# Performance work log

Hardware: AMD Instinct MI355X
Metric: run time of the kernel (lower is better)

The kernel has to match this reference:

```python
import jax, jax.numpy as jnp
import numpy as np

EPS = 1e-8
MIN_VAL = -1e7  # module default min_val=-10000000.0


def _div_safe(n, d):
    return n / jnp.maximum(d, EPS)


def _cosine_pairwise(v1, v2):
    # v1: (B,L1,H), v2: (B,L2,H) -> (B,L1,L2)
    n1 = jnp.linalg.norm(v1, axis=2, keepdims=True)
    n2 = jnp.linalg.norm(v2, axis=2, keepdims=True)
    a = jnp.einsum('bik,bjk->bij', v1, v2)
    return _div_safe(a, n1 * jnp.swapaxes(n2, 1, 2))


def _masked_max(v, mask, axis, keepdims=False):
    rep = jnp.where(mask > 0, v, MIN_VAL)
    val = jnp.max(rep, axis=axis, keepdims=keepdims)
    m = jnp.max(jnp.broadcast_to(mask, v.shape), axis=axis, keepdims=keepdims)
    return val * m


def _masked_mean(v, mask, axis, keepdims=False):
    s = jnp.sum(v * mask, axis=axis, keepdims=keepdims)
    c = jnp.sum(jnp.broadcast_to(mask, v.shape), axis=axis, keepdims=keepdims)
    return _div_safe(s, c)


def _cos_sim(a, b, axis):
    # torch F.cosine_similarity semantics: dot / (max(|a|,eps)*max(|b|,eps))
    dot = jnp.sum(a * b, axis=axis)
    na = jnp.maximum(jnp.linalg.norm(a, axis=axis), EPS)
    nb = jnp.maximum(jnp.linalg.norm(b, axis=axis), EPS)
    return dot / (na * nb)


def _mpm(v1, v2, w):
    # v1, v2: (B,L,H); w: (P,H) -> ((B,L,1), (B,L,P))
    mv1 = _cos_sim(v1, v2, 2)[..., None]
    v1w = w[None, None] * v1[:, :, None, :]  # (B,L,P,H)
    v2w = w[None, None] * v2[:, :, None, :]
    return mv1, _cos_sim(v1w, v2w, 3)


def _mpm_pairwise(v1, v2, w):
    # v1: (B,L1,H), v2: (B,L2,H), w: (P,H) -> (B,L1,L2,P)
    v1w = w[None, :, None, :] * v1[:, None, :, :]  # (B,P,L1,H)
    v2w = w[None, :, None, :] * v2[:, None, :, :]  # (B,P,L2,H)
    n1 = jnp.linalg.norm(v1w, axis=3, keepdims=True)
    n2 = jnp.linalg.norm(v2w, axis=3, keepdims=True)
    n = jnp.einsum('bpik,bpjk->bpij', v1w, v2w)
    d = n1 * jnp.swapaxes(n2, 2, 3)
    return jnp.transpose(_div_safe(n, d), (0, 2, 3, 1))


def setup_inputs() -> dict:
    key = jax.random.key(0)
    ks = jax.random.split(key, 8)
    B, L, H, P = 32, 128, 100, 20
    return {
        'context_p': jax.random.normal(ks[0], (B, L, H), dtype=jnp.float32),
        'mask_p': jax.random.randint(ks[1], (B, L), 0, 2, dtype=jnp.int32),
        'context_h': jax.random.normal(ks[2], (B, L, H), dtype=jnp.float32),
        'mask_h': jax.random.randint(ks[3], (B, L), 0, 2, dtype=jnp.int32),
        'w0': jax.random.uniform(ks[4], (P, H), dtype=jnp.float32),
        'w1': jax.random.uniform(ks[5], (P, H), dtype=jnp.float32),
        'w2': jax.random.uniform(ks[6], (P, H), dtype=jnp.float32),
        'w3': jax.random.uniform(ks[7], (P, H), dtype=jnp.float32),
    }


def reference(context_p, mask_p, context_h, mask_h, w0, w1, w2, w3):
    mask_p = mask_p.astype(jnp.float32)
    mask_h = mask_h.astype(jnp.float32)
    B, Lp, H = context_p.shape
    Lh = context_h.shape[1]

    mask_p_h = mask_p[:, :, None] * mask_h[:, None, :]   # (B,Lp,Lh)
    mask_h_p = jnp.swapaxes(mask_p_h, 1, 2)              # (B,Lh,Lp)
    cp = context_p * mask_p[..., None]
    ch = context_h * mask_h[..., None]

    # --- pairwise cosine + masked max/mean pooling ---
    cos = _cosine_pairwise(cp, ch)                        # (B,Lp,Lh)
    cosT = jnp.swapaxes(cos, 1, 2)
    cos_max_p = _masked_max(cos, mask_p_h, 2, True)
    cos_mean_p = _masked_mean(cos, mask_p_h, 2, True)
    cos_max_h = _masked_max(cosT, mask_h_p, 2, True)
    cos_mean_h = _masked_mean(cosT, mask_h_p, 2, True)

    # --- full match (is_forward=True: last real token) ---
    idx_p = jnp.clip(jnp.sum(mask_p, 1).astype(jnp.int32) - 1, 0)[:, None, None]
    idx_h = jnp.clip(jnp.sum(mask_h, 1).astype(jnp.int32) - 1, 0)[:, None, None]
    cp_last = jnp.take_along_axis(cp, jnp.broadcast_to(idx_p, (B, 1, H)), axis=1)
    ch_last = jnp.take_along_axis(ch, jnp.broadcast_to(idx_h, (B, 1, H)), axis=1)
    mv_p_f1, mv_p_fP = _mpm(cp, jnp.broadcast_to(ch_last, (B, Lp, H)), w0)
    mv_h_f1, mv_h_fP = _mpm(ch, jnp.broadcast_to(cp_last, (B, Lh, H)), w0)

    # --- maxpool match ---
    mv_max = _mpm_pairwise(cp, ch, w1)                    # (B,Lp,Lh,P)
    mv_p_max = _masked_max(mv_max, mask_p_h[..., None], 2)
    mv_p_mean = _masked_mean(mv_max, mask_p_h[..., None], 2)
    mv_maxT = jnp.transpose(mv_max, (0, 2, 1, 3))
    mv_h_max = _masked_max(mv_maxT, mask_h_p[..., None], 2)
    mv_h_mean = _masked_mean(mv_maxT, mask_h_p[..., None], 2)

    # --- attentive match (mean) ---
    att_mean_h = _div_safe(jnp.einsum('bij,bjh->bih', cos, ch),
                           jnp.sum(cos, 2, keepdims=True))
    att_mean_p = _div_safe(jnp.einsum('bij,bih->bjh', cos, cp),
                           jnp.swapaxes(jnp.sum(cos, 1, keepdims=True), 1, 2))
    mv_p_am1, mv_p_amP = _mpm(cp, att_mean_h, w2)
    mv_h_am1, mv_h_amP = _mpm(ch, att_mean_p, w2)

    # --- max-attentive match ---
    att_h = ch[:, None, :, :] * cos[:, :, :, None]        # (B,Lp,Lh,H)
    att_p_t = cp[:, None, :, :] * cosT[:, :, :, None]     # (B,Lh,Lp,H) == att_p.permute(0,2,1,3)
    att_max_h = _masked_max(att_h, mask_p_h[..., None], 2)
    att_max_p = _masked_max(att_p_t, mask_h_p[..., None], 2)
    mv_p_ax1, mv_p_axP = _mpm(cp, att_max_h, w3)
    mv_h_ax1, mv_h_axP = _mpm(ch, att_max_p, w3)

    mv_p = jnp.concatenate([cos_max_p, cos_mean_p, mv_p_f1, mv_p_fP,
                            mv_p_max, mv_p_mean, mv_p_am1, mv_p_amP,
                            mv_p_ax1, mv_p_axP], axis=2)
    mv_h = jnp.concatenate([cos_max_h, cos_mean_h, mv_h_f1, mv_h_fP,
                            mv_h_max, mv_h_mean, mv_h_am1, mv_h_amP,
                            mv_h_ax1, mv_h_axP], axis=2)
    return mv_p, mv_h
```

## Files before the change

kernel.cpp:

```cpp
#include <hip/hip_runtime.h>
#include <math.h>


namespace {
constexpr int B = 32;
constexpr int L = 128;
constexpr int H = 100;
constexpr int P = 20;
constexpr int C = 105;
constexpr int TI = 8;
constexpr int SMEM_BYTES = 50176;
constexpr float EPSF = 1e-8f;
constexpr float MINV = -1e7f;
}

typedef unsigned short u16;
typedef unsigned int u32;
typedef short sh8 __attribute__((ext_vector_type(8)));
typedef float f4 __attribute__((ext_vector_type(4)));

__device__ __forceinline__ u16 f2bf(float f) {
    u32 u = __float_as_uint(f);
    u += 0x7FFFu + ((u >> 16) & 1u);
    return (u16)(u >> 16);
}
__device__ __forceinline__ float bf2f(u32 h) {
    return __uint_as_float(h << 16);
}
__device__ __forceinline__ u32 pack2(float a, float b) {
    return (u32)f2bf(a) | ((u32)f2bf(b) << 16);
}

__global__ void k_prep(const float* __restrict__ ctx_p, const int* __restrict__ mask_p,
                       const float* __restrict__ ctx_h, const int* __restrict__ mask_h,
                       const float* __restrict__ w1,
                       float* __restrict__ cp, float* __restrict__ ch,
                       u16* __restrict__ cpb, u16* __restrict__ chb,
                       float* __restrict__ np_, float* __restrict__ nh_,
                       float* __restrict__ nwp, float* __restrict__ nwh)
{
    const int b = blockIdx.y, i = blockIdx.x, side = blockIdx.z, t = threadIdx.x;
    const float* ctx = side ? ctx_h : ctx_p;
    const int*  mask = side ? mask_h : mask_p;
    float* dst  = side ? ch  : cp;
    u16*   dstb = side ? chb : cpb;
    float* nrm  = side ? nh_ : np_;
    float* nw   = side ? nwh : nwp;

    const int row = b * L + i;
    __shared__ __align__(16) float sv2[H];
    const float m = (float)mask[row];
    float v = 0.f;
    if (t < H) {
        v = ctx[row * H + t] * m;
        dst[row * H + t] = v;
        sv2[t] = v * v;
    }
    dstb[row * 128 + t] = f2bf(v);
    __syncthreads();

    const int w = t >> 6, ln = t & 63;
    int g = -1, seg = 0;
    if (w == 0) { if (ln < 60) { g = ln / 5; seg = ln % 5; } }
    else        { if (ln < 45) { g = 12 + ln / 5; seg = ln % 5; } }
    if (g >= 0) {
        const float4* v4 = (const float4*)sv2;
        float acc = 0.f;
        if (g < P) {
            const float4* w4 = (const float4*)(w1 + g * H);
            #pragma unroll
            for (int k = seg * 5; k < seg * 5 + 5; ++k) {
                float4 wv_ = w4[k], s = v4[k];
                acc += wv_.x * wv_.x * s.x + wv_.y * wv_.y * s.y +
                       wv_.z * wv_.z * s.z + wv_.w * wv_.w * s.w;
            }
        } else {
            #pragma unroll
            for (int k = seg * 5; k < seg * 5 + 5; ++k) {
                float4 s = v4[k];
                acc += s.x + s.y + s.z + s.w;
            }
        }
        float a1 = __shfl(acc, ln + 1), a2 = __shfl(acc, ln + 2);
        float a3 = __shfl(acc, ln + 3), a4 = __shfl(acc, ln + 4);
        if (seg == 0) {
            float s = acc + a1 + a2 + a3 + a4;
            if (g < P) nw[row * P + g] = sqrtf(s);
            else       nrm[row] = sqrtf(s);
        }
    }
}

__global__ __launch_bounds__(512) void
k_main(const float* __restrict__ cp, const float* __restrict__ ch,
       const u16* __restrict__ cpb, const u16* __restrict__ chb,
       const float* __restrict__ np_, const float* __restrict__ nh_,
       const float* __restrict__ nw1p, const float* __restrict__ nw1h,
       const int* __restrict__ mask_p, const int* __restrict__ mask_h,
       const float* __restrict__ w0, const float* __restrict__ w1,
       const float* __restrict__ w2, const float* __restrict__ w3,
       float* __restrict__ out)
{
    __shared__ __align__(16) char smem[SMEM_BYTES];
    const int bx = blockIdx.x, b = blockIdx.y, t = threadIdx.x;
    const int wv = t >> 6, ln = t & 63;
    float* out_p = out;
    float* out_h = out + (size_t)B * L * C;

    if (bx < P) {
        const int p = bx;
        u16*  sB    = (u16*)smem;
        float* snwA = (float*)(smem + 34816);
        float* snwB = (float*)(smem + 35328);
        float* smA  = (float*)(smem + 35840);
        float* smB  = (float*)(smem + 36352);
        float* pJmax= (float*)(smem + 36864);
        float* pJsum= (float*)(smem + 37376);
        float* pImax= (float*)(smem + 37888);
        float* pIsum= (float*)(smem + 41984);
        float* sRed = (float*)(smem + 46080);

        if (t < 128) {
            snwA[t] = nw1p[(b * L + t) * P + p];
            snwB[t] = nw1h[(b * L + t) * P + p];
            smA[t] = (float)mask_p[b * L + t];
            smB[t] = (float)mask_h[b * L + t];
        }
        __syncthreads();

        if (t < 64) {
            float a0 = smB[t], a1 = smB[t + 64];
            float mx = fmaxf(a0, a1), sm = a0 + a1;
            for (int d = 1; d < 64; d <<= 1) {
                mx = fmaxf(mx, __shfl_xor(mx, d));
                sm += __shfl_xor(sm, d);
            }
            if (t == 0) { sRed[2] = mx; sRed[3] = sm; }
        } else if (t < 128) {
            const int l = t - 64;
            float a0 = smA[l], a1 = smA[l + 64];
            float mx = fmaxf(a0, a1), sm = a0 + a1;
            for (int d = 1; d < 64; d <<= 1) {
                mx = fmaxf(mx, __shfl_xor(mx, d));
                sm += __shfl_xor(sm, d);
            }
            if (l == 0) { sRed[0] = mx; sRed[1] = sm; }
        }

        {
            const uint4* src = (const uint4*)(chb + (size_t)b * L * 128);
            #pragma unroll
            for (int it = 0; it < 4; ++it) {
                int idx = it * 512 + t;
                int row = idx >> 4, kc = (idx & 15) * 8;
                uint4 v = src[idx];
                *(uint4*)&sB[row * 136 + kc] = v;
            }
        }
        __syncthreads();

        const int m = ln & 15, q = ln >> 4;

        float swv[4][8];
        #pragma unroll
        for (int ks = 0; ks < 4; ++ks)
            #pragma unroll
            for (int e = 0; e < 8; ++e) {
                int k = ks * 32 + q * 8 + e;
                float w = (k < H) ? w1[p * H + k] : 0.f;
                swv[ks][e] = w * w;
            }

        f4 acc[8];
        #pragma unroll
        for (int ct = 0; ct < 8; ++ct) acc[ct] = (f4){0.f, 0.f, 0.f, 0.f};

        const uint4* gA = (const uint4*)(cpb + (size_t)(b * L + wv * 16 + m) * 128);

        #pragma unroll
        for (int ks = 0; ks < 4; ++ks) {
            uint4 va = gA[ks * 4 + q];
            sh8 af;
            {
                u32 vs[4] = {va.x, va.y, va.z, va.w};
                u32 r[4];
                #pragma unroll
                for (int e = 0; e < 4; ++e) {
                    float f0 = bf2f(vs[e] & 0xffffu) * swv[ks][2 * e];
                    float f1 = bf2f(vs[e] >> 16) * swv[ks][2 * e + 1];
                    r[e] = (u32)f2bf(f0) | ((u32)f2bf(f1) << 16);
                }
                uint4 o = {r[0], r[1], r[2], r[3]};
                af = __builtin_bit_cast(sh8, o);
            }
            const int ko = ks * 32 + q * 8;
            #pragma unroll
            for (int ct = 0; ct < 8; ++ct) {
                sh8 bb = *(const sh8*)&sB[(ct * 16 + m) * 136 + ko];
                acc[ct] = __builtin_amdgcn_mfma_f32_16x16x32_bf16(af, bb, acc[ct], 0, 0, 0);
            }
        }

        float nB[8], mBv[8], imax[8], isum[8];
        #pragma unroll
        for (int ct = 0; ct < 8; ++ct) {
            const int j = ct * 16 + m;
            nB[ct] = snwB[j]; mBv[ct] = smB[j];
            imax[ct] = MINV; isum[ct] = 0.f;
        }
        #pragma unroll
        for (int reg = 0; reg < 4; ++reg) {
            const int i = wv * 16 + q * 4 + reg;
            const float na = snwA[i];
            const float ma = smA[i];
            float jmax = MINV, jsum = 0.f;
            #pragma unroll
            for (int ct = 0; ct < 8; ++ct) {
                float v = acc[ct][reg] *
                          __builtin_amdgcn_rcpf(fmaxf(na * nB[ct], EPSF));
                jmax = fmaxf(jmax, mBv[ct] > 0.f ? v : MINV);
                jsum += mBv[ct] > 0.f ? v : 0.f;
                imax[ct] = fmaxf(imax[ct], ma > 0.f ? v : MINV);
                isum[ct] += ma > 0.f ? v : 0.f;
            }
            for (int d = 1; d < 16; d <<= 1) {
                jmax = fmaxf(jmax, __shfl_xor(jmax, d));
                jsum += __shfl_xor(jsum, d);
            }
            if (m == 0) { pJmax[i] = jmax; pJsum[i] = jsum; }
        }
        #pragma unroll
        for (int ct = 0; ct < 8; ++ct) {
            float mx = imax[ct], sm = isum[ct];
            mx = fmaxf(mx, __shfl_xor(mx, 16)); sm += __shfl_xor(sm, 16);
            mx = fmaxf(mx, __shfl_xor(mx, 32)); sm += __shfl_xor(sm, 32);
            if (q == 0) { const int j = ct * 16 + m; pImax[wv * 128 + j] = mx; pIsum[wv * 128 + j] = sm; }
        }
        __syncthreads();

        if (t < 128) {
            const int i = t;
            const float ma = smA[i];
            const float mm = ma * sRed[2];
            const float cnt = ma * sRed[3];
            float* orow = out_p + ((size_t)b * L + i) * C;
            orow[23 + p] = pJmax[i] * mm;
            orow[43 + p] = ma * pJsum[i] / fmaxf(cnt, EPSF);

            const float mb = smB[i];
            float hmax = MINV, hsum = 0.f;
            #pragma unroll
            for (int s = 0; s < 8; ++s) {
                hmax = fmaxf(hmax, pImax[s * 128 + i]);
                hsum += pIsum[s * 128 + i];
            }
            float* hrow = out_h + ((size_t)b * L + i) * C;
            hrow[23 + p] = hmax * mb * sRed[0];
            hrow[43 + p] = mb * hsum / fmaxf(mb * sRed[1], EPSF);
        }
    } else {
        const int e = bx - P;
        const int side = e >> 4, tile = e & 15;
        const int i0 = tile * TI;
        const float* A   = side ? ch : cp;
        const float* Bv  = side ? cp : ch;
        const u16*  Ab16 = side ? chb : cpb;
        const u16*  Bvb  = side ? cpb : chb;
        const float* nA_ = side ? nh_ : np_;
        const float* nB_ = side ? np_ : nh_;
        const int* maskA = side ? mask_h : mask_p;
        const int* maskB = side ? mask_p : mask_h;
        float* outBase = out + ((size_t)side * B * L + (size_t)b * L) * C;

        float* scosC = (float*)(smem + 34816);
        float* sa    = (float*)(smem + 38912);
        float* sam   = (float*)(smem + 42496);
        float* sax   = (float*)(smem + 46080);
        float* sl    = (float*)(smem + 49664);
        float* snB   = (float*)(smem + 42496);
        float* snA   = (float*)(smem + 43008);
        u16*  cidx  = (u16*)(smem + 43040);
        int*   pnv   = (int*)(smem + 50112);

        scosC[t] = 0.f;
        scosC[t + 512] = 0.f;
        if (wv == 0) {
            int m0 = maskB[b * L + ln], m1 = maskB[b * L + 64 + ln];
            unsigned long long b0 = __ballot(m0 > 0);
            unsigned long long b1 = __ballot(m1 > 0);
            unsigned long long pre = (1ull << ln) - 1ull;
            int n0 = __popcll(b0);
            if (m0 > 0) cidx[__popcll(b0 & pre)] = (u16)ln;
            if (m1 > 0) cidx[n0 + __popcll(b1 & pre)] = (u16)(64 + ln);
            if (ln == 0) *pnv = n0 + __popcll(b1);
        } else if (wv >= 2) {
            for (int x = t - 128; x < TI * 128; x += 384) {
                int il = x >> 7, k = x & 127;
                if (k < H) sa[il * 112 + k] = A[((size_t)b * L + i0 + il) * H + k];
            }
        }
        __syncthreads();
        const int nv = *pnv;
        const int nct = (nv + 15) >> 4;

        {
            const uint4* src = (const uint4*)(Bvb + (size_t)b * L * 128);
            for (int c = t; c < nct * 256; c += 512) {
                int jj = c >> 4, cc = c & 15;
                uint4 v;
                if (jj < nv) v = src[(int)cidx[jj] * 16 + cc];
                else { v.x = v.y = v.z = v.w = 0u; }
                *(uint4*)(smem + jj * 272 + cc * 16) = v;
            }
            if (t < 128) snB[t] = (t < nv) ? nB_[b * L + (int)cidx[t]] : 0.f;
            else if (t < 136) snA[t - 128] = nA_[b * L + i0 + (t - 128)];
            if (wv == 1) {
                int last = nv - 1; if (last < 0) last = 0;
                const float* lr = Bv + ((size_t)b * L + last) * H;
                sl[ln] = lr[ln];
                if (ln + 64 < H) sl[ln + 64] = lr[ln + 64];
            }
        }
        __syncthreads();

        const int m = ln & 15, q = ln >> 4;
        if (wv < nct) {
            const uint4* gA = (const uint4*)(Ab16 + (size_t)(b * L + i0 + (m & 7)) * 128);
            f4 acc0 = (f4){0.f, 0.f, 0.f, 0.f};
            #pragma unroll
            for (int ks = 0; ks < 4; ++ks) {
                uint4 va = gA[ks * 4 + q];
                if (m >= 8) { va.x = va.y = va.z = va.w = 0u; }
                sh8 af = __builtin_bit_cast(sh8, va);
                const int ko2 = (ks * 32 + q * 8) * 2;
                sh8 bb = *(const sh8*)(smem + (wv * 16 + m) * 272 + ko2);
                acc0 = __builtin_amdgcn_mfma_f32_16x16x32_bf16(af, bb, acc0, 0, 0, 0);
            }
            if (q < 2) {
                #pragma unroll
                for (int reg = 0; reg < 4; ++reg) {
                    const int i = q * 4 + reg;
                    const int jj = wv * 16 + m;
                    scosC[i * 128 + jj] = acc0[reg] *
                        __builtin_amdgcn_rcpf(fmaxf(snA[i] * snB[jj], EPSF));
                }
            }
        }
        __syncthreads();

        {
            const int il = wv;
            const int gi = i0 + il;
            const float mA = (float)maskA[b * L + gi];
            float c0 = scosC[il * 128 + ln], c1 = scosC[il * 128 + 64 + ln];
            float scj = c0 + c1;
            float mv0 = (ln < nv) ? c0 : MINV;
            float mv1 = (ln + 64 < nv) ? c1 : MINV;
            float cmx = fmaxf(mv0, mv1);
            for (int d = 1; d < 64; d <<= 1) {
                scj += __shfl_xor(scj, d);
                cmx = fmaxf(cmx, __shfl_xor(cmx, d));
            }
            const float mm = (nv > 0) ? mA : 0.f;
            if (ln == 0) {
                float* orow = outBase + (size_t)gi * C;
                orow[0] = cmx * mm;
                orow[1] = mA * scj / fmaxf(mA * (float)nv, EPSF);
            }
            if (ln < 50) {
                float am0 = 0.f, am1 = 0.f, ax0 = MINV, ax1 = MINV;
                const u32* bp = (const u32*)smem + ln;
                const float* cr = scosC + il * 128;
                #pragma unroll 4
                for (int jj = 0; jj < nv; ++jj) {
                    u32 pk = bp[jj * 68];
                    float cj = cr[jj];
                    float v0 = cj * __uint_as_float(pk << 16);
                    float v1 = cj * __uint_as_float(pk & 0xffff0000u);
                    am0 += v0; am1 += v1;
                    ax0 = fmaxf(ax0, v0); ax1 = fmaxf(ax1, v1);
                }
                const float rs = __builtin_amdgcn_rcpf(fmaxf(scj, EPSF));
                sam[il * 112 + 2 * ln] = am0 * rs; sam[il * 112 + 2 * ln + 1] = am1 * rs;
                sax[il * 112 + 2 * ln] = ax0 * mm; sax[il * 112 + 2 * ln + 1] = ax1 * mm;
            }
        }
        __syncthreads();

        for (int idx = t; idx < 8 * 8 * 17; idx += 512) {
            int kc = (idx % 17) * 8;
            int tmp = idx / 17;
            int il = tmp >> 3, col = tmp & 7;
            const float* sa_il  = sa  + il * 112;
            const float* sam_il = sam + il * 112;
            const float* sax_il = sax + il * 112;
            const float* p1 = (col >= 4) ? (col == 4 ? sl : col == 5 ? sam_il : sax_il)
                                         : sa_il;
            const float* p2 = (col == 0 || col == 4) ? sl :
                              (col == 1 || col == 5) ? sam_il :
                              (col == 2 || col == 6) ? sax_il : sa_il;
            u32 ow[4];
            #pragma unroll
            for (int e2 = 0; e2 < 4; ++e2) {
                int k0 = kc + 2 * e2;
                float f0 = (col < 7 && k0 < H)     ? p1[k0] * p2[k0]         : 0.f;
                float f1 = (col < 7 && k0 + 1 < H) ? p1[k0 + 1] * p2[k0 + 1] : 0.f;
                ow[e2] = pack2(f0, f1);
            }
            uint4 o = {ow[0], ow[1], ow[2], ow[3]};
            *(uint4*)(smem + (tmp * 136 + kc) * 2) = o;
        }
        for (int idx = t; idx < 64 * 17; idx += 512) {
            int kc = (idx % 17) * 8;
            int row = idx / 17;
            u32 ow[4];
            #pragma unroll
            for (int e2 = 0; e2 < 4; ++e2) {
                int k0 = kc + 2 * e2;
                float f0 = 0.f, f1 = 0.f;
                if (row < 60) {
                    const float* wr = (row < 20) ? w0 + row * H :
                                      (row < 40) ? w2 + (row - 20) * H :
                                                   w3 + (row - 40) * H;
                    if (k0 < H)     { float w = wr[k0];     f0 = w * w; }
                    if (k0 + 1 < H) { float w = wr[k0 + 1]; f1 = w * w; }
                } else if (row == 60) {
                    f0 = (k0 < H) ? 1.f : 0.f;
                    f1 = (k0 + 1 < H) ? 1.f : 0.f;
                }
                ow[e2] = pack2(f0, f1);
            }
            uint4 o = {ow[0], ow[1], ow[2], ow[3]};
            *(uint4*)(smem + 17408 + (row * 136 + kc) * 2) = o;
        }
        __syncthreads();

        f4 d3[4];
        #pragma unroll
        for (int Mt = 0; Mt < 4; ++Mt) d3[Mt] = (f4){0.f, 0.f, 0.f, 0.f};
        {
            const int cn = m & 7;
            #pragma unroll
            for (int ks = 0; ks < 4; ++ks) {
                const int ko2 = (ks * 32 + q * 8) * 2;
                sh8 bb = *(const sh8*)(smem + ((wv * 8 + cn) * 136) * 2 + ko2);
                #pragma unroll
                for (int Mt = 0; Mt < 4; ++Mt) {
                    sh8 aa = *(const sh8*)(smem + 17408 + ((Mt * 16 + m) * 136) * 2 + ko2);
                    d3[Mt] = __builtin_amdgcn_mfma_f32_16x16x32_bf16(aa, bb, d3[Mt], 0, 0, 0);
                }
            }
        }
        __syncthreads();

        if (m < 8) {
            #pragma unroll
            for (int Mt = 0; Mt < 4; ++Mt)
                #pragma unroll
                for (int reg = 0; reg < 4; ++reg)
                    ((float*)smem)[wv * 512 + (Mt * 16 + q * 4 + reg) * 8 + m] = d3[Mt][reg];
        }
        __syncthreads();

        for (int task = t; task < TI * 63; task += 512) {
            const int il = task / 63, c = task - il * 63;
            int row, dcol, nbcol, chn;
            if (c < 60) {
                const int grp = c / 20;
                row = c; dcol = grp; nbcol = 4 + grp;
                chn = ((grp == 0) ? 3 : (grp == 1) ? 64 : 85) + (c - grp * 20);
            } else {
                const int cc = c - 60;
                row = 60; dcol = cc; nbcol = 4 + cc;
                chn = (cc == 0) ? 2 : (cc == 1) ? 63 : 84;
            }
            const float* Dr = (const float*)smem + il * 512 + row * 8;
            float d = Dr[dcol], na = Dr[3], nb = Dr[nbcol];
            outBase[(size_t)(i0 + il) * C + chn] =
                d / (fmaxf(sqrtf(na), EPSF) * fmaxf(sqrtf(nb), EPSF));
        }
    }
}

extern "C" void kernel_launch(void* const* d_in, const int* in_sizes, int n_in,
                              void* d_out, int out_size, void* d_ws, size_t ws_size,
                              hipStream_t stream)
{
    const float* ctx_p = (const float*)d_in[0];
    const int*   mask_p = (const int*)d_in[1];
    const float* ctx_h = (const float*)d_in[2];
    const int*   mask_h = (const int*)d_in[3];
    const float* w0 = (const float*)d_in[4];
    const float* w1 = (const float*)d_in[5];
    const float* w2 = (const float*)d_in[6];
    const float* w3 = (const float*)d_in[7];
    float* out = (float*)d_out;

    float* ws   = (float*)d_ws;
    float* cp   = ws;
    float* ch   = cp   + B * L * H;
    float* np_  = ch   + B * L * H;
    float* nh_  = np_  + B * L;
    float* nw1p = nh_  + B * L;
    float* nw1h = nw1p + B * L * P;
    u16*   cpb  = (u16*)(nw1h + B * L * P);
    u16*   chb  = cpb + B * L * 128;

    k_prep<<<dim3(L, B, 2), dim3(128), 0, stream>>>(
        ctx_p, mask_p, ctx_h, mask_h, w1,
        cp, ch, cpb, chb, np_, nh_, nw1p, nw1h);
    k_main<<<dim3(P + 32, B), dim3(512), 0, stream>>>(
        cp, ch, cpb, chb, np_, nh_, nw1p, nw1h, mask_p, mask_h,
        w0, w1, w2, w3, out);
}
```

Baseline: 124.0 us.

## Fuse preprocessing kernel into main kernel, computing masks, norms and bf16 packing inline

Removes the separate k_prep launch and its workspace round trip. The main kernel now reads the raw contexts and masks directly, applies the mask, computes row norms and weighted norms, and converts to bf16 on the fly. This saves one launch and the global writes and reads of the intermediates. In exchange, the norms and conversions are recomputed redundantly across the 20 p-blocks and the 32 tile blocks. The shared-memory stride for the final D buffer is also padded from 8 to 9, apparently to reduce bank conflicts.

New measurement: 126.1 us. No clear change (+1.6%).

```diff
diff --git a/kernel.cpp b/kernel.cpp
--- a/kernel.cpp
+++ b/kernel.cpp
@@ -24,79 +24,20 @@
     u += 0x7FFFu + ((u >> 16) & 1u);
     return (u16)(u >> 16);
 }
-__device__ __forceinline__ float bf2f(u32 h) {
-    return __uint_as_float(h << 16);
-}
 __device__ __forceinline__ u32 pack2(float a, float b) {
     return (u32)f2bf(a) | ((u32)f2bf(b) << 16);
 }
-
-__global__ void k_prep(const float* __restrict__ ctx_p, const int* __restrict__ mask_p,
-                       const float* __restrict__ ctx_h, const int* __restrict__ mask_h,
-                       const float* __restrict__ w1,
-                       float* __restrict__ cp, float* __restrict__ ch,
-                       u16* __restrict__ cpb, u16* __restrict__ chb,
-                       float* __restrict__ np_, float* __restrict__ nh_,
-                       float* __restrict__ nwp, float* __restrict__ nwh)
-{
-    const int b = blockIdx.y, i = blockIdx.x, side = blockIdx.z, t = threadIdx.x;
-    const float* ctx = side ? ctx_h : ctx_p;
-    const int*  mask = side ? mask_h : mask_p;
-    float* dst  = side ? ch  : cp;
-    u16*   dstb = side ? chb : cpb;
-    float* nrm  = side ? nh_ : np_;
-    float* nw   = side ? nwh : nwp;
-
-    const int row = b * L + i;
-    __shared__ __align__(16) float sv2[H];
-    const float m = (float)mask[row];
-    float v = 0.f;
-    if (t < H) {
-        v = ctx[row * H + t] * m;
-        dst[row * H + t] = v;
-        sv2[t] = v * v;
-    }
-    dstb[row * 128 + t] = f2bf(v);
-    __syncthreads();
-
-    const int w = t >> 6, ln = t & 63;
-    int g = -1, seg = 0;
-    if (w == 0) { if (ln < 60) { g = ln / 5; seg = ln % 5; } }
-    else        { if (ln < 45) { g = 12 + ln / 5; seg = ln % 5; } }
-    if (g >= 0) {
-        const float4* v4 = (const float4*)sv2;
-        float acc = 0.f;
-        if (g < P) {
-            const float4* w4 = (const float4*)(w1 + g * H);
-            #pragma unroll
-            for (int k = seg * 5; k < seg * 5 + 5; ++k) {
-                float4 wv_ = w4[k], s = v4[k];
-                acc += wv_.x * wv_.x * s.x + wv_.y * wv_.y * s.y +
-                       wv_.z * wv_.z * s.z + wv_.w * wv_.w * s.w;
-            }
-        } else {
-            #pragma unroll
-            for (int k = seg * 5; k < seg * 5 + 5; ++k) {
-                float4 s = v4[k];
-                acc += s.x + s.y + s.z + s.w;
-            }
-        }
-        float a1 = __shfl(acc, ln + 1), a2 = __shfl(acc, ln + 2);
-        float a3 = __shfl(acc, ln + 3), a4 = __shfl(acc, ln + 4);
-        if (seg == 0) {
-            float s = acc + a1 + a2 + a3 + a4;
-            if (g < P) nw[row * P + g] = sqrtf(s);
-            else       nrm[row] = sqrtf(s);
-        }
-    }
-}
+__device__ __forceinline__ uint4 pack8(const float4 h0, const float4 h1) {
+    uint4 o;
+    o.x = pack2(h0.x, h0.y); o.y = pack2(h0.z, h0.w);
+    o.z = pack2(h1.x, h1.y); o.w = pack2(h1.z, h1.w);
+    return o;
+}
+__device__ __forceinline__ float4 zero4() { return (float4){0.f, 0.f, 0.f, 0.f}; }
 
 __global__ __launch_bounds__(512) void
-k_main(const float* __restrict__ cp, const float* __restrict__ ch,
-       const u16* __restrict__ cpb, const u16* __restrict__ chb,
-       const float* __restrict__ np_, const float* __restrict__ nh_,
-       const float* __restrict__ nw1p, const float* __restrict__ nw1h,
-       const int* __restrict__ mask_p, const int* __restrict__ mask_h,
+k_main(const float* __restrict__ ctx_p, const int* __restrict__ mask_p,
+       const float* __restrict__ ctx_h, const int* __restrict__ mask_h,
        const float* __restrict__ w0, const float* __restrict__ w1,
        const float* __restrict__ w2, const float* __restrict__ w3,
        float* __restrict__ out)
@@ -119,15 +60,44 @@
         float* pImax= (float*)(smem + 37888);
         float* pIsum= (float*)(smem + 41984);
         float* sRed = (float*)(smem + 46080);
-
-        if (t < 128) {
-            snwA[t] = nw1p[(b * L + t) * P + p];
-            snwB[t] = nw1h[(b * L + t) * P + p];
-            smA[t] = (float)mask_p[b * L + t];
-            smB[t] = (float)mask_h[b * L + t];
-        }
-        __syncthreads();
-
+        float* sw1sq= (float*)(smem + 46096);
+
+        if (t < 128) smA[t] = (float)mask_p[b * L + t];
+        else if (t < 256) smB[t - 128] = (float)mask_h[b * L + (t - 128)];
+        else if (t < 384) {
+            int k = t - 256;
+            float w = (k < H) ? w1[p * H + k] : 0.f;
+            sw1sq[k] = w * w;
+        }
+        __syncthreads();
+
+        if (t < 256) {
+            const int sideSel = t >> 7, rr = t & 127;
+            const float* rowp = (sideSel ? ctx_h : ctx_p) + ((size_t)b * L + rr) * H;
+            const float mrow = sideSel ? smB[rr] : smA[rr];
+            const float4* r4 = (const float4*)rowp;
+            float acc = 0.f;
+            #pragma unroll 5
+            for (int k4 = 0; k4 < 25; ++k4) {
+                float4 v = r4[k4];
+                const float* wq = sw1sq + k4 * 4;
+                float v0 = v.x * mrow, v1 = v.y * mrow, v2 = v.z * mrow, v3 = v.w * mrow;
+                acc += wq[0] * v0 * v0 + wq[1] * v1 * v1 +
+                       wq[2] * v2 * v2 + wq[3] * v3 * v3;
+            }
+            (sideSel ? snwB : snwA)[rr] = sqrtf(acc);
+        } else {
+            for (int idx = t - 256; idx < 2048; idx += 256) {
+                int row = idx >> 4, c = idx & 15, k0 = c * 8;
+                const float* rowp = ctx_h + ((size_t)b * L + row) * H;
+                float mrow = smB[row];
+                float4 h0 = (k0 <= 96) ? *(const float4*)(rowp + k0) : zero4();
+                float4 h1 = (k0 + 4 <= 96) ? *(const float4*)(rowp + k0 + 4) : zero4();
+                h0.x *= mrow; h0.y *= mrow; h0.z *= mrow; h0.w *= mrow;
+                h1.x *= mrow; h1.y *= mrow; h1.z *= mrow; h1.w *= mrow;
+                *(uint4*)&sB[row * 136 + k0] = pack8(h0, h1);
+            }
+        }
         if (t < 64) {
             float a0 = smB[t], a1 = smB[t + 64];
             float mx = fmaxf(a0, a1), sm = a0 + a1;
@@ -146,17 +116,6 @@
             }
             if (l == 0) { sRed[0] = mx; sRed[1] = sm; }
         }
-
-        {
-            const uint4* src = (const uint4*)(chb + (size_t)b * L * 128);
-            #pragma unroll
-            for (int it = 0; it < 4; ++it) {
-                int idx = it * 512 + t;
-                int row = idx >> 4, kc = (idx & 15) * 8;
-                uint4 v = src[idx];
-                *(uint4*)&sB[row * 136 + kc] = v;
-            }
-        }
         __syncthreads();
 
         const int m = ln & 15, q = ln >> 4;
@@ -167,37 +126,37 @@
             #pragma unroll
             for (int e = 0; e < 8; ++e) {
                 int k = ks * 32 + q * 8 + e;
-                float w = (k < H) ? w1[p * H + k] : 0.f;
-                swv[ks][e] = w * w;
+                swv[ks][e] = (k < H) ? sw1sq[k] : 0.f;
             }
 
         f4 acc[8];
         #pragma unroll
         for (int ct = 0; ct < 8; ++ct) acc[ct] = (f4){0.f, 0.f, 0.f, 0.f};
 
-        const uint4* gA = (const uint4*)(cpb + (size_t)(b * L + wv * 16 + m) * 128);
-
-        #pragma unroll
-        for (int ks = 0; ks < 4; ++ks) {
-            uint4 va = gA[ks * 4 + q];
-            sh8 af;
-            {
-                u32 vs[4] = {va.x, va.y, va.z, va.w};
-                u32 r[4];
+        {
+            const int arow = wv * 16 + m;
+            const float* rowp = ctx_p + ((size_t)b * L + arow) * H;
+            const float mA = smA[arow];
+            #pragma unroll
+            for (int ks = 0; ks < 4; ++ks) {
+                const int k0 = ks * 32 + q * 8;
+                float4 h0 = (k0 <= 96) ? *(const float4*)(rowp + k0) : zero4();
+                float4 h1 = (k0 + 4 <= 96) ? *(const float4*)(rowp + k0 + 4) : zero4();
+                sh8 af;
+                {
+                    uint4 o;
+                    o.x = pack2(h0.x * mA * swv[ks][0], h0.y * mA * swv[ks][1]);
+                    o.y = pack2(h0.z * mA * swv[ks][2], h0.w * mA * swv[ks][3]);
+                    o.z = pack2(h1.x * mA * swv[ks][4], h1.y * mA * swv[ks][5]);
+                    o.w = pack2(h1.z * mA * swv[ks][6], h1.w * mA * swv[ks][7]);
+                    af = __builtin_bit_cast(sh8, o);
+                }
+                const int ko = ks * 32 + q * 8;
                 #pragma unroll
-                for (int e = 0; e < 4; ++e) {
-                    float f0 = bf2f(vs[e] & 0xffffu) * swv[ks][2 * e];
-                    float f1 = bf2f(vs[e] >> 16) * swv[ks][2 * e + 1];
-                    r[e] = (u32)f2bf(f0) | ((u32)f2bf(f1) << 16);
-                }
-                uint4 o = {r[0], r[1], r[2], r[3]};
-                af = __builtin_bit_cast(sh8, o);
-            }
-            const int ko = ks * 32 + q * 8;
-            #pragma unroll
-            for (int ct = 0; ct < 8; ++ct) {
-                sh8 bb = *(const sh8*)&sB[(ct * 16 + m) * 136 + ko];
-                acc[ct] = __builtin_amdgcn_mfma_f32_16x16x32_bf16(af, bb, acc[ct], 0, 0, 0);
+                for (int ct = 0; ct < 8; ++ct) {
+                    sh8 bb = *(const sh8*)&sB[(ct * 16 + m) * 136 + ko];
+                    acc[ct] = __builtin_amdgcn_mfma_f32_16x16x32_bf16(af, bb, acc[ct], 0, 0, 0);
+                }
             }
         }
 
@@ -262,12 +221,8 @@
         const int e = bx - P;
         const int side = e >> 4, tile = e & 15;
         const int i0 = tile * TI;
-        const float* A   = side ? ch : cp;
-        const float* Bv  = side ? cp : ch;
-        const u16*  Ab16 = side ? chb : cpb;
-        const u16*  Bvb  = side ? cpb : chb;
-        const float* nA_ = side ? nh_ : np_;
-        const float* nB_ = side ? np_ : nh_;
+        const float* ctxA = side ? ctx_h : ctx_p;
+        const float* ctxB = side ? ctx_p : ctx_h;
         const int* maskA = side ? mask_h : mask_p;
         const int* maskB = side ? mask_p : mask_h;
         float* outBase = out + ((size_t)side * B * L + (size_t)b * L) * C;
@@ -296,7 +251,10 @@
         } else if (wv >= 2) {
             for (int x = t - 128; x < TI * 128; x += 384) {
                 int il = x >> 7, k = x & 127;
-                if (k < H) sa[il * 112 + k] = A[((size_t)b * L + i0 + il) * H + k];
+                if (k < H) {
+                    float mA = (float)maskA[b * L + i0 + il];
+                    sa[il * 112 + k] = ctxA[((size_t)b * L + i0 + il) * H + k] * mA;
+                }
             }
         }
         __syncthreads();
@@ -304,35 +262,72 @@
         const int nct = (nv + 15) >> 4;
 
         {
-            const uint4* src = (const uint4*)(Bvb + (size_t)b * L * 128);
             for (int c = t; c < nct * 256; c += 512) {
-                int jj = c >> 4, cc = c & 15;
-                uint4 v;
-                if (jj < nv) v = src[(int)cidx[jj] * 16 + cc];
-                else { v.x = v.y = v.z = v.w = 0u; }
-                *(uint4*)(smem + jj * 272 + cc * 16) = v;
-            }
-            if (t < 128) snB[t] = (t < nv) ? nB_[b * L + (int)cidx[t]] : 0.f;
-            else if (t < 136) snA[t - 128] = nA_[b * L + i0 + (t - 128)];
+                int jj = c >> 4, cc = c & 15, k0 = cc * 8;
+                uint4 o;
+                if (jj < nv) {
+                    const float* rowp = ctxB + ((size_t)b * L + (int)cidx[jj]) * H;
+                    float4 h0 = (k0 <= 96) ? *(const float4*)(rowp + k0) : zero4();
+                    float4 h1 = (k0 + 4 <= 96) ? *(const float4*)(rowp + k0 + 4) : zero4();
+                    o = pack8(h0, h1);
+                } else { o.x = o.y = o.z = o.w = 0u; }
+                *(uint4*)(smem + jj * 272 + k0 * 2) = o;
+            }
+            {
+                const int jj = t >> 2, quarter = t & 3;
+                float acc = 0.f;
+                if (jj < nv) {
+                    const float* rowp = ctxB + ((size_t)b * L + (int)cidx[jj]) * H;
+                    #pragma unroll 5
+                    for (int k = quarter * 25; k < quarter * 25 + 25; ++k) {
+                        float v = rowp[k];
+                        acc += v * v;
+                    }
+                }
+                acc += __shfl_xor(acc, 1);
+                acc += __shfl_xor(acc, 2);
+                if (quarter == 0) snB[jj] = (jj < nv) ? sqrtf(acc) : 0.f;
+            }
+            if (t < 32) {
+                const int il = t >> 2, quarter = t & 3;
+                float acc = 0.f;
+                #pragma unroll 5
+                for (int k = quarter * 25; k < quarter * 25 + 25; ++k) {
+                    float v = sa[il * 112 + k];
+                    acc += v * v;
+                }
+                acc += __shfl_xor(acc, 1);
+                acc += __shfl_xor(acc, 2);
+                if (quarter == 0) snA[il] = sqrtf(acc);
+            }
             if (wv == 1) {
                 int last = nv - 1; if (last < 0) last = 0;
-                const float* lr = Bv + ((size_t)b * L + last) * H;
-                sl[ln] = lr[ln];
-                if (ln + 64 < H) sl[ln + 64] = lr[ln + 64];
+                const float mLast = (float)maskB[b * L + last];
+                const float* lr = ctxB + ((size_t)b * L + last) * H;
+                sl[ln] = lr[ln] * mLast;
+                if (ln + 64 < H) sl[ln + 64] = lr[ln + 64] * mLast;
             }
         }
         __syncthreads();
 
         const int m = ln & 15, q = ln >> 4;
         if (wv < nct) {
-            const uint4* gA = (const uint4*)(Ab16 + (size_t)(b * L + i0 + (m & 7)) * 128);
+            const int il8 = m & 7;
+            const float* rowp = ctxA + ((size_t)b * L + i0 + il8) * H;
+            const float mA = (m < 8) ? (float)maskA[b * L + i0 + il8] : 0.f;
             f4 acc0 = (f4){0.f, 0.f, 0.f, 0.f};
             #pragma unroll
             for (int ks = 0; ks < 4; ++ks) {
-                uint4 va = gA[ks * 4 + q];
-                if (m >= 8) { va.x = va.y = va.z = va.w = 0u; }
-                sh8 af = __builtin_bit_cast(sh8, va);
-                const int ko2 = (ks * 32 + q * 8) * 2;
+                const int k0 = ks * 32 + q * 8;
+                float4 h0 = (k0 <= 96) ? *(const float4*)(rowp + k0) : zero4();
+                float4 h1 = (k0 + 4 <= 96) ? *(const float4*)(rowp + k0 + 4) : zero4();
+                uint4 o;
+                o.x = pack2(h0.x * mA, h0.y * mA);
+                o.y = pack2(h0.z * mA, h0.w * mA);
+                o.z = pack2(h1.x * mA, h1.y * mA);
+                o.w = pack2(h1.z * mA, h1.w * mA);
+                sh8 af = __builtin_bit_cast(sh8, o);
+                const int ko2 = k0 * 2;
                 sh8 bb = *(const sh8*)(smem + (wv * 16 + m) * 272 + ko2);
                 acc0 = __builtin_amdgcn_mfma_f32_16x16x32_bf16(af, bb, acc0, 0, 0, 0);
             }
@@ -458,7 +453,7 @@
             for (int Mt = 0; Mt < 4; ++Mt)
                 #pragma unroll
                 for (int reg = 0; reg < 4; ++reg)
-                    ((float*)smem)[wv * 512 + (Mt * 16 + q * 4 + reg) * 8 + m] = d3[Mt][reg];
+                    ((float*)smem)[wv * 576 + (Mt * 16 + q * 4 + reg) * 9 + m] = d3[Mt][reg];
         }
         __syncthreads();
 
@@ -474,7 +469,7 @@
                 row = 60; dcol = cc; nbcol = 4 + cc;
                 chn = (cc == 0) ? 2 : (cc == 1) ? 63 : 84;
             }
-            const float* Dr = (const float*)smem + il * 512 + row * 8;
+            const float* Dr = (const float*)smem + il * 576 + row * 9;
             float d = Dr[dcol], na = Dr[3], nb = Dr[nbcol];
             outBase[(size_t)(i0 + il) * C + chn] =
                 d / (fmaxf(sqrtf(na), EPSF) * fmaxf(sqrtf(nb), EPSF));
@@ -495,21 +490,8 @@
     const float* w2 = (const float*)d_in[6];
     const float* w3 = (const float*)d_in[7];
     float* out = (float*)d_out;
-
-    float* ws   = (float*)d_ws;
-    float* cp   = ws;
-    float* ch   = cp   + B * L * H;
-    float* np_  = ch   + B * L * H;
-    float* nh_  = np_  + B * L;
-    float* nw1p = nh_  + B * L;
-    float* nw1h = nw1p + B * L * P;
-    u16*   cpb  = (u16*)(nw1h + B * L * P);
-    u16*   chb  = cpb + B * L * 128;
-
-    k_prep<<<dim3(L, B, 2), dim3(128), 0, stream>>>(
-        ctx_p, mask_p, ctx_h, mask_h, w1,
-        cp, ch, cpb, chb, np_, nh_, nw1p, nw1h);
+    (void)d_ws; (void)ws_size;
+
     k_main<<<dim3(P + 32, B), dim3(512), 0, stream>>>(
-        cp, ch, cpb, chb, np_, nh_, nw1p, nw1h, mask_p, mask_h,
-        w0, w1, w2, w3, out);
-}
+        ctx_p, mask_p, ctx_h, mask_h, w0, w1, w2, w3, out);
+}
```
